# Performance work log

Measured on AMD Instinct MI355X. Metric: run time of the kernel, lower is better.

Reference implementation:

```python
import jax, jax.numpy as jnp
import numpy as np

N = 50000      # nodes
E = 800000     # edges
F = 128        # num_features
H = 128        # hidden_channels
L = 3          # num_layers
P = 32         # num_partitions
EPS = 1e-5     # BatchNorm1d eps


def _batchnorm(h):
    # BatchNorm1d(affine=False, track_running_stats=False): batch stats, biased var
    m = jnp.mean(h, axis=0)
    v = jnp.var(h, axis=0)
    return (h - m) * jax.lax.rsqrt(v + EPS)


def setup_inputs() -> dict:
    key = jax.random.key(0)
    ks = jax.random.split(key, 12)
    x = jax.random.normal(ks[0], (N, F), dtype=jnp.float32)
    edge_index = jax.random.randint(ks[1], (2, E), 0, N)
    edge_weights = jax.random.uniform(ks[2], (E,), dtype=jnp.float32)
    partitions = (jax.random.uniform(ks[3], (N, P)) < (1.0 / P)).astype(jnp.float32)
    node_weights = jax.random.uniform(ks[4], (N,), dtype=jnp.float32)
    edge_curr_node = jax.random.uniform(ks[5], (N,), dtype=jnp.float32)
    conv_w = 0.05 * jax.random.normal(ks[6], (L, F, H), dtype=jnp.float32)
    conv_b = jnp.zeros((L, H), dtype=jnp.float32)
    lin1_w = 0.05 * jax.random.normal(ks[7], (4 * H, H), dtype=jnp.float32)
    lin1_b = jnp.zeros((H,), dtype=jnp.float32)
    lin2_w = 0.05 * jax.random.normal(ks[8], (H, 1), dtype=jnp.float32)
    lin2_b = jnp.zeros((1,), dtype=jnp.float32)
    return {"x": x, "edge_index": edge_index, "edge_weights": edge_weights,
            "partitions": partitions, "node_weights": node_weights,
            "edge_curr_node": edge_curr_node, "conv_w": conv_w, "conv_b": conv_b,
            "lin1_w": lin1_w, "lin1_b": lin1_b, "lin2_w": lin2_w,
            "lin2_b": lin2_b, "curr_node_id": 123}


def reference(x, edge_index, edge_weights, partitions, node_weights,
              edge_curr_node, conv_w, conv_b, lin1_w, lin1_b, lin2_w, lin2_b,
              curr_node_id):
    src, dst = edge_index[0], edge_index[1]
    # GCN normalization with added self-loops (weight 1)
    deg = jax.ops.segment_sum(edge_weights, dst, num_segments=N) + 1.0
    dinv = jax.lax.rsqrt(deg)
    norm = dinv[src] * edge_weights * dinv[dst]          # [E]
    self_norm = (dinv * dinv)[:, None]                   # [N,1]

    h = x
    for l in range(L):
        hw = h @ conv_w[l] + conv_b[l]                   # [N,H]
        agg = jax.ops.segment_sum(hw[src] * norm[:, None], dst, num_segments=N)
        agg = agg + hw * self_norm                       # self-loop term
        h = jax.nn.relu(_batchnorm(agg))

    x_curr = h[curr_node_id]                             # [H]
    # mlp scoring: concat [h | x_curr | edge_col repeated to 2H] -> [N,4H]
    cat = jnp.concatenate([
        h,
        jnp.broadcast_to(x_curr[None, :], (N, H)),
        jnp.broadcast_to(edge_curr_node[:, None], (N, 2 * H)),
    ], axis=1)
    scores = jax.nn.relu(cat @ lin1_w + lin1_b) @ lin2_w + lin2_b  # [N,1]
    # pool == 'sum'
    partition_scores = scores.T @ partitions             # [1,P]
    return (partition_scores, h)
```

## Files before the change

kernel.cpp:

```cpp
#include <hip/hip_runtime.h>

#define N_NODES 50000
#define N_EDGES 800000
#define NP 50048
#define BKT 784
#define NBKT 64
#define BREG 16384
#define HB 782
#define PADK 136
#define NCOPY 64
#define WPB 512

typedef __bf16 bf16_8 __attribute__((ext_vector_type(8)));
typedef float  f32_4  __attribute__((ext_vector_type(4)));

__device__ inline float2 bf2f2(unsigned int u) {
    union { unsigned int i; float f; } a, b;
    a.i = u << 16;
    b.i = u & 0xffff0000u;
    return make_float2(a.f, b.f);
}

__global__ void k_init_wprep(float* __restrict__ colpart, float* __restrict__ out_head,
                             int* __restrict__ cursor,
                             const float* __restrict__ conv_w, const float* __restrict__ lin1_w,
                             __bf16* __restrict__ WT, float* __restrict__ svec) {
    int b = blockIdx.x;
    if (b < 64) {
        int i = b * 256 + threadIdx.x;
        colpart[i] = 0.f;
        if (i < 32) out_head[i] = 0.f;
        if (i < NBKT) cursor[i] = 0;
    } else if (b < 64 + WPB) {
        int b2 = b - 64;
        int mat = b2 >> 7, n = b2 & 127, k = threadIdx.x;
        if (k < 128) {
            const float* srcm = (mat < 3) ? (conv_w + (size_t)mat * 16384) : lin1_w;
            WT[((size_t)mat * 128 + n) * 128 + k] = (__bf16)srcm[(size_t)k * 128 + n];
        }
    } else {
        int j = threadIdx.x;
        if (j < 128) {
            float s = 0.f;
            for (int k = 256; k < 512; ++k) s += lin1_w[(size_t)k * 128 + j];
            svec[j] = s;
        }
    }
}

__global__ __launch_bounds__(256) void k_scatter(const int* __restrict__ src,
                                                 const int* __restrict__ dst,
                                                 const float* __restrict__ ew,
                                                 int* __restrict__ cursor,
                                                 uint2* __restrict__ ebuf) {
    __shared__ int c[NBKT], basee[NBKT];
    int t = threadIdx.x, b = blockIdx.x;
    if (t < NBKT) c[t] = 0;
    __syncthreads();
    int e0 = b * 1024;
    int myd[4], mybkt[4];
#pragma unroll
    for (int j = 0; j < 4; ++j) {
        int e = e0 + t + j * 256;
        mybkt[j] = -1;
        if (e < N_EDGES) {
            myd[j] = dst[e];
            mybkt[j] = myd[j] / BKT;
            atomicAdd(&c[mybkt[j]], 1);
        }
    }
    __syncthreads();
    if (t < NBKT && c[t] > 0) basee[t] = atomicAdd(&cursor[t], c[t]);
    __syncthreads();
    if (t < NBKT) c[t] = 0;
    __syncthreads();
#pragma unroll
    for (int j = 0; j < 4; ++j) {
        if (mybkt[j] >= 0) {
            int e = e0 + t + j * 256;
            int bkt = mybkt[j];
            int dl = myd[j] - bkt * BKT;
            int pos = basee[bkt] + atomicAdd(&c[bkt], 1);
            ebuf[(size_t)bkt * BREG + pos] =
                make_uint2(((unsigned)dl << 17) | (unsigned)src[e], __float_as_uint(ew[e]));
        }
    }
}

__global__ __launch_bounds__(256) void k_build(const uint2* __restrict__ ebuf,
                                               const int* __restrict__ cursor,
                                               uint2* __restrict__ esn2,
                                               int* __restrict__ offs, int* __restrict__ cnt,
                                               float* __restrict__ dinv) {
    __shared__ int   c784[1024];
    __shared__ float deg784[1024];
    __shared__ int   o784[1024];
    __shared__ int   fill784[1024];
    __shared__ int   p[256];
    int b = blockIdx.x, t = threadIdx.x;
    size_t base = (size_t)b * BREG;
    int num = cursor[b];
    for (int i = t; i < 1024; i += 256) { c784[i] = 0; deg784[i] = 1.0f; fill784[i] = 0; }
    __syncthreads();
    for (int i = t; i < num; i += 256) {
        uint2 eu = ebuf[base + i];
        int dl = eu.x >> 17;
        atomicAdd(&c784[dl], 1);
        atomicAdd(&deg784[dl], __uint_as_float(eu.y));
    }
    __syncthreads();
    for (int i = t; i < BKT; i += 256) deg784[i] = rsqrtf(deg784[i]);
    int s0 = c784[4 * t] + c784[4 * t + 1] + c784[4 * t + 2] + c784[4 * t + 3];
    p[t] = s0;
    __syncthreads();
    int own = s0;
    for (int d = 1; d < 256; d <<= 1) {
        int v = (t >= d) ? p[t - d] : 0;
        __syncthreads();
        p[t] += v;
        __syncthreads();
    }
    int e0 = p[t] - own;
    o784[4 * t] = e0;
    o784[4 * t + 1] = e0 + c784[4 * t];
    o784[4 * t + 2] = e0 + c784[4 * t] + c784[4 * t + 1];
    o784[4 * t + 3] = e0 + c784[4 * t] + c784[4 * t + 1] + c784[4 * t + 2];
    __syncthreads();
    int nb0 = b * BKT;
    for (int i = t; i < BKT; i += 256) {
        int n = nb0 + i;
        if (n < N_NODES) {
            offs[n] = (int)base + o784[i];
            cnt[n] = c784[i];
            dinv[n] = deg784[i];
        }
    }
    __syncthreads();
    for (int i = t; i < num; i += 256) {
        uint2 eu = ebuf[base + i];
        int dl = eu.x >> 17;
        int s  = (int)(eu.x & 131071u);
        int pos = (int)base + o784[dl] + atomicAdd(&fill784[dl], 1);
        esn2[pos] = make_uint2((unsigned)s,
                               __float_as_uint(__uint_as_float(eu.y) * deg784[dl]));
    }
}

template <int AMODE>
__global__ __launch_bounds__(256) void k_gemm_mfma(const float* __restrict__ A,
                                                   const float* __restrict__ mean,
                                                   const float* __restrict__ rstd,
                                                   const __bf16* __restrict__ WT,
                                                   const float* __restrict__ bias,
                                                   __bf16* __restrict__ C, int nrows) {
    __shared__ __bf16 As[64 * PADK];
    __shared__ __bf16 Ws[128 * PADK];
    int t = threadIdx.x;
    int rowBase = blockIdx.x * 64;
    const uint4* WTg = (const uint4*)WT;
    for (int i = t; i < 2048; i += 256) {
        int n = i >> 4, k8 = i & 15;
        *(uint4*)&Ws[n * PADK + k8 * 8] = WTg[i];
    }
    const float4* A4 = (const float4*)A;
    const float4* M4 = (const float4*)mean;
    const float4* R4 = (const float4*)rstd;
    for (int i = t; i < 1024; i += 256) {
        int r = i >> 4, k8 = i & 15;
        int gr = rowBase + r;
        float4 a0 = make_float4(0.f, 0.f, 0.f, 0.f), a1 = a0;
        if (gr < nrows) {
            a0 = A4[(size_t)gr * 32 + k8 * 2];
            a1 = A4[(size_t)gr * 32 + k8 * 2 + 1];
        }
        if (AMODE == 1) {
            float4 m0 = M4[k8 * 2], m1 = M4[k8 * 2 + 1];
            float4 r0 = R4[k8 * 2], r1 = R4[k8 * 2 + 1];
            a0.x = fmaxf((a0.x - m0.x) * r0.x, 0.f); a0.y = fmaxf((a0.y - m0.y) * r0.y, 0.f);
            a0.z = fmaxf((a0.z - m0.z) * r0.z, 0.f); a0.w = fmaxf((a0.w - m0.w) * r0.w, 0.f);
            a1.x = fmaxf((a1.x - m1.x) * r1.x, 0.f); a1.y = fmaxf((a1.y - m1.y) * r1.y, 0.f);
            a1.z = fmaxf((a1.z - m1.z) * r1.z, 0.f); a1.w = fmaxf((a1.w - m1.w) * r1.w, 0.f);
        }
        bf16_8 o = { (__bf16)a0.x, (__bf16)a0.y, (__bf16)a0.z, (__bf16)a0.w,
                     (__bf16)a1.x, (__bf16)a1.y, (__bf16)a1.z, (__bf16)a1.w };
        *(bf16_8*)&As[r * PADK + k8 * 8] = o;
    }
    __syncthreads();
    int wave = t >> 6, lane = t & 63, quad = lane >> 4, m = lane & 15;
    int ar = wave * 16 + m;
    f32_4 acc[8];
#pragma unroll
    for (int i = 0; i < 8; ++i) acc[i] = (f32_4){0.f, 0.f, 0.f, 0.f};
#pragma unroll
    for (int kk = 0; kk < 4; ++kk) {
        bf16_8 a = *(const bf16_8*)&As[ar * PADK + kk * 32 + quad * 8];
#pragma unroll
        for (int n0 = 0; n0 < 8; ++n0) {
            bf16_8 b = *(const bf16_8*)&Ws[(n0 * 16 + m) * PADK + kk * 32 + quad * 8];
            acc[n0] = __builtin_amdgcn_mfma_f32_16x16x32_bf16(a, b, acc[n0], 0, 0, 0);
        }
    }
    __syncthreads();
#pragma unroll
    for (int n0 = 0; n0 < 8; ++n0) {
        int col = n0 * 16 + m;
        float bi = bias[col];
#pragma unroll
        for (int r = 0; r < 4; ++r) {
            int rr = wave * 16 + quad * 4 + r;
            As[rr * PADK + col] = (__bf16)(acc[n0][r] + bi);
        }
    }
    __syncthreads();
    uint4* Cg = (uint4*)C;
    for (int i = t; i < 1024; i += 256) {
        int r = i >> 4, k8 = i & 15;
        int gr = rowBase + r;
        if (gr < nrows) Cg[(size_t)gr * 16 + k8] = *(const uint4*)&As[r * PADK + k8 * 8];
    }
}

__global__ __launch_bounds__(256) void k_agg(const __bf16* __restrict__ hwb,
                                             const uint2* __restrict__ esn2,
                                             const int* __restrict__ offs,
                                             const int* __restrict__ cnt,
                                             const float* __restrict__ dinv,
                                             float* __restrict__ agg,
                                             float* __restrict__ colpart) {
    __shared__ float red1[4 * 128], red2[4 * 128];
    int t = threadIdx.x;
    int n = (blockIdx.x * 256 + t) >> 6;
    int lane = t & 63, wave = t >> 6;
    float2 acc = make_float2(0.f, 0.f);
    const unsigned int* hw32 = (const unsigned int*)hwb;
    if (n < N_NODES) {
        float dvn = dinv[n];
        float2 sv = bf2f2(hw32[(size_t)n * 64 + lane]);
        acc.x = sv.x * dvn * dvn; acc.y = sv.y * dvn * dvn;
        int beg = offs[n], num = cnt[n];
        for (int ch = 0; ch < num; ch += 64) {
            int nn = min(64, num - ch);
            int s_l = 0; float w_l = 0.f;
            if (lane < nn) {
                uint2 e = esn2[beg + ch + lane];
                s_l = (int)e.x;
                w_l = dinv[s_l] * __uint_as_float(e.y);
            }
            int i = 0;
            for (; i + 8 <= nn; i += 8) {
                int ss[8]; float ww[8]; unsigned uu[8];
#pragma unroll
                for (int j = 0; j < 8; ++j) { ss[j] = __shfl(s_l, i + j); ww[j] = __shfl(w_l, i + j); }
#pragma unroll
                for (int j = 0; j < 8; ++j) uu[j] = hw32[(size_t)ss[j] * 64 + lane];
#pragma unroll
                for (int j = 0; j < 8; ++j) {
                    float2 f = bf2f2(uu[j]);
                    acc.x += f.x * ww[j]; acc.y += f.y * ww[j];
                }
            }
            for (; i < nn; ++i) {
                int s = __shfl(s_l, i);
                float w = __shfl(w_l, i);
                float2 f = bf2f2(hw32[(size_t)s * 64 + lane]);
                acc.x += f.x * w; acc.y += f.y * w;
            }
        }
        ((float2*)agg)[(size_t)n * 64 + lane] = acc;
    }
    *(float2*)&red1[wave * 128 + 2 * lane] = acc;
    *(float2*)&red2[wave * 128 + 2 * lane] = make_float2(acc.x * acc.x, acc.y * acc.y);
    __syncthreads();
    if (t < 128) {
        float s = red1[t] + red1[128 + t] + red1[256 + t] + red1[384 + t];
        float q = red2[t] + red2[128 + t] + red2[256 + t] + red2[384 + t];
        int c = blockIdx.x & (NCOPY - 1);
        unsafeAtomicAdd(&colpart[c * 128 + t], s);
        unsafeAtomicAdd(&colpart[NCOPY * 128 + c * 128 + t], q);
    }
}

template <int DO_PREP>
__global__ void k_bnfinal(float* __restrict__ colpart, float* __restrict__ mean,
                          float* __restrict__ rstd,
                          const float* __restrict__ agg, const int* __restrict__ cid,
                          const float* __restrict__ lin1w, const float* __restrict__ lin1b,
                          float* __restrict__ c0) {
    __shared__ float s1[256], s2[256], ms[128], rs[128], xc[128];
    int t = threadIdx.x;
    int j = t & 127, g = t >> 7;
    float s = 0.f, q = 0.f;
    for (int c = g * 32; c < g * 32 + 32; ++c) {
        s += colpart[c * 128 + j];
        q += colpart[NCOPY * 128 + c * 128 + j];
        colpart[c * 128 + j] = 0.f;
        colpart[NCOPY * 128 + c * 128 + j] = 0.f;
    }
    s1[t] = s; s2[t] = q;
    __syncthreads();
    if (t < 128) {
        float S = s1[t] + s1[t + 128];
        float Q = s2[t] + s2[t + 128];
        float m = S * (1.0f / N_NODES);
        float v = Q * (1.0f / N_NODES) - m * m;
        float r = rsqrtf(v + 1e-5f);
        mean[t] = m; rstd[t] = r;
        if (DO_PREP) { ms[t] = m; rs[t] = r; }
    }
    if (DO_PREP) {
        __syncthreads();
        int cn = cid[0];
        if (t < 128) xc[t] = fmaxf((agg[(size_t)cn * 128 + t] - ms[t]) * rs[t], 0.f);
        __syncthreads();
        float acc = g ? 0.f : lin1b[j];
        for (int k = g * 64; k < g * 64 + 64; ++k)
            acc += xc[k] * lin1w[(size_t)(128 + k) * 128 + j];
        s1[t] = acc;
        __syncthreads();
        if (t < 128) c0[t] = s1[t] + s1[t + 128];
    }
}

__global__ __launch_bounds__(256) void k_score_mfma(const float* __restrict__ agg,
                                                    const float* __restrict__ mean,
                                                    const float* __restrict__ rstd,
                                                    const __bf16* __restrict__ WT,
                                                    const float* __restrict__ c0,
                                                    const float* __restrict__ svec,
                                                    const float* __restrict__ ecn,
                                                    const float* __restrict__ lin2w,
                                                    const float* __restrict__ lin2b,
                                                    const float* __restrict__ part,
                                                    float* __restrict__ out,
                                                    float* __restrict__ hout,
                                                    int nrows) {
    __shared__ __bf16 As[64 * PADK];
    __shared__ __bf16 Ws[128 * PADK];
    __shared__ float c0s[128], svs[128], l2s[128];
    __shared__ float sc[64], red[256];
    int t = threadIdx.x;
    int rowBase = blockIdx.x * 64;
    const uint4* WTg = (const uint4*)WT;
    for (int i = t; i < 2048; i += 256) {
        int n = i >> 4, k8 = i & 15;
        *(uint4*)&Ws[n * PADK + k8 * 8] = WTg[i];
    }
    const float4* A4 = (const float4*)agg;
    const float4* M4 = (const float4*)mean;
    const float4* R4 = (const float4*)rstd;
    float4* H4 = (float4*)hout;
    for (int i = t; i < 1024; i += 256) {
        int r = i >> 4, k8 = i & 15;
        int gr = rowBase + r;
        float4 a0 = make_float4(0.f, 0.f, 0.f, 0.f), a1 = a0;
        if (gr < nrows) {
            a0 = A4[(size_t)gr * 32 + k8 * 2];
            a1 = A4[(size_t)gr * 32 + k8 * 2 + 1];
        }
        float4 m0 = M4[k8 * 2], m1 = M4[k8 * 2 + 1];
        float4 r0 = R4[k8 * 2], r1 = R4[k8 * 2 + 1];
        float4 f0, f1;
        f0.x = fmaxf((a0.x - m0.x) * r0.x, 0.f); f0.y = fmaxf((a0.y - m0.y) * r0.y, 0.f);
        f0.z = fmaxf((a0.z - m0.z) * r0.z, 0.f); f0.w = fmaxf((a0.w - m0.w) * r0.w, 0.f);
        f1.x = fmaxf((a1.x - m1.x) * r1.x, 0.f); f1.y = fmaxf((a1.y - m1.y) * r1.y, 0.f);
        f1.z = fmaxf((a1.z - m1.z) * r1.z, 0.f); f1.w = fmaxf((a1.w - m1.w) * r1.w, 0.f);
        if (gr < nrows) {
            H4[(size_t)gr * 32 + k8 * 2] = f0;
            H4[(size_t)gr * 32 + k8 * 2 + 1] = f1;
        }
        bf16_8 o = { (__bf16)f0.x, (__bf16)f0.y, (__bf16)f0.z, (__bf16)f0.w,
                     (__bf16)f1.x, (__bf16)f1.y, (__bf16)f1.z, (__bf16)f1.w };
        *(bf16_8*)&As[r * PADK + k8 * 8] = o;
    }
    if (t < 128) { c0s[t] = c0[t]; svs[t] = svec[t]; l2s[t] = lin2w[t]; }
    __syncthreads();
    int wave = t >> 6, lane = t & 63, quad = lane >> 4, m = lane & 15;
    int ar = wave * 16 + m;
    f32_4 acc[8];
#pragma unroll
    for (int i = 0; i < 8; ++i) acc[i] = (f32_4){0.f, 0.f, 0.f, 0.f};
#pragma unroll
    for (int kk = 0; kk < 4; ++kk) {
        bf16_8 a = *(const bf16_8*)&As[ar * PADK + kk * 32 + quad * 8];
#pragma unroll
        for (int n0 = 0; n0 < 8; ++n0) {
            bf16_8 b = *(const bf16_8*)&Ws[(n0 * 16 + m) * PADK + kk * 32 + quad * 8];
            acc[n0] = __builtin_amdgcn_mfma_f32_16x16x32_bf16(a, b, acc[n0], 0, 0, 0);
        }
    }
    float l2b = lin2b[0];
#pragma unroll
    for (int r = 0; r < 4; ++r) {
        int row = rowBase + wave * 16 + quad * 4 + r;
        float e = (row < nrows) ? ecn[row] : 0.f;
        float partial = 0.f;
#pragma unroll
        for (int n0 = 0; n0 < 8; ++n0) {
            int col = n0 * 16 + m;
            float v = acc[n0][r] + c0s[col] + e * svs[col];
            partial += fmaxf(v, 0.f) * l2s[col];
        }
        partial += __shfl_xor(partial, 8, 16);
        partial += __shfl_xor(partial, 4, 16);
        partial += __shfl_xor(partial, 2, 16);
        partial += __shfl_xor(partial, 1, 16);
        if (m == 0) sc[wave * 16 + quad * 4 + r] = partial + l2b;
    }
    __syncthreads();
    int rg = t >> 5, pp = t & 31;
    float a = 0.f;
    for (int j = 0; j < 8; ++j) {
        int r = rg * 8 + j;
        int row = rowBase + r;
        if (row < nrows) a += sc[r] * part[(size_t)row * 32 + pp];
    }
    red[t] = a;
    __syncthreads();
    if (t < 32) {
        float s = 0.f;
        for (int i = 0; i < 8; ++i) s += red[i * 32 + t];
        unsafeAtomicAdd(&out[t], s);
    }
}

extern "C" void kernel_launch(void* const* d_in, const int* in_sizes, int n_in,
                              void* d_out, int out_size, void* d_ws, size_t ws_size,
                              hipStream_t stream) {
    const float* x        = (const float*)d_in[0];
    const int*   eidx     = (const int*)d_in[1];
    const float* ew       = (const float*)d_in[2];
    const float* parts    = (const float*)d_in[3];
    const float* ecn      = (const float*)d_in[5];
    const float* conv_w   = (const float*)d_in[6];
    const float* conv_b   = (const float*)d_in[7];
    const float* lin1_w   = (const float*)d_in[8];
    const float* lin1_b   = (const float*)d_in[9];
    const float* lin2_w   = (const float*)d_in[10];
    const float* lin2_b   = (const float*)d_in[11];
    const int*   cid      = (const int*)d_in[12];

    const int* src = eidx;
    const int* dst = eidx + N_EDGES;

    char* p = (char*)d_ws;
    auto alloc = [&](size_t bytes) { char* r = p; p += (bytes + 255) & ~size_t(255); return r; };
    int*    cursor  = (int*)alloc(NBKT * 4);
    uint2*  ebuf    = (uint2*)alloc((size_t)NBKT * BREG * 8);
    uint2*  esn2    = (uint2*)alloc((size_t)NBKT * BREG * 8);
    int*    offs    = (int*)alloc(NP * 4);
    int*    cnt     = (int*)alloc(NP * 4);
    float*  dinv    = (float*)alloc(NP * 4);
    float*  colpart = (float*)alloc(2 * NCOPY * 128 * 4);
    float*  mean    = (float*)alloc(128 * 4);
    float*  rstd    = (float*)alloc(128 * 4);
    float*  c0      = (float*)alloc(128 * 4);
    float*  svec    = (float*)alloc(128 * 4);
    __bf16* WT      = (__bf16*)alloc(4 * 128 * 128 * 2);
    __bf16* hwb     = (__bf16*)alloc((size_t)N_NODES * 128 * 2);
    float*  agg     = (float*)alloc((size_t)N_NODES * 128 * 4);

    float* out_head = (float*)d_out;
    float* hbuf     = (float*)d_out + 32;

    const int GB = (N_NODES + 63) / 64;
    const int AB = (N_NODES * 64 + 255) / 256;

    k_init_wprep<<<64 + WPB + 1, 256, 0, stream>>>(colpart, out_head, cursor,
                                                   conv_w, lin1_w, WT, svec);
    k_scatter<<<HB, 256, 0, stream>>>(src, dst, ew, cursor, ebuf);
    k_build<<<NBKT, 256, 0, stream>>>(ebuf, cursor, esn2, offs, cnt, dinv);

    for (int l = 0; l < 3; ++l) {
        if (l == 0)
            k_gemm_mfma<0><<<GB, 256, 0, stream>>>(x, mean, rstd, WT, conv_b, hwb, N_NODES);
        else
            k_gemm_mfma<1><<<GB, 256, 0, stream>>>(agg, mean, rstd, WT + (size_t)l * 16384,
                                                   conv_b + (size_t)l * 128, hwb, N_NODES);
        k_agg<<<AB, 256, 0, stream>>>(hwb, esn2, offs, cnt, dinv, agg, colpart);
        if (l < 2)
            k_bnfinal<0><<<1, 256, 0, stream>>>(colpart, mean, rstd,
                                                agg, cid, lin1_w, lin1_b, c0);
        else
            k_bnfinal<1><<<1, 256, 0, stream>>>(colpart, mean, rstd,
                                                agg, cid, lin1_w, lin1_b, c0);
    }

    k_score_mfma<<<GB, 256, 0, stream>>>(agg, mean, rstd, WT + (size_t)3 * 16384, c0, svec,
                                         ecn, lin2_w, lin2_b, parts, out_head, hbuf, N_NODES);
}
```

Measured before the change: 373.5 us.

## Halve edge bucket size and stage sorted CSR edges in shared memory

Edges are now split into 128 destination buckets of 392 nodes instead of 64 of 784, which doubles the number of build blocks for more parallelism. The sorted edge records are staged in LDS and written to global memory in coalesced order instead of being scattered. The lin1 column-sum prep is split across two thread groups. Bucket overflow past BREG is now silently clamped, which drops edges if a bucket exceeds 8192 entries.

New measurement: 358.1 us. -4.1%, faster.

```diff
diff --git a/kernel.cpp b/kernel.cpp
--- a/kernel.cpp
+++ b/kernel.cpp
@@ -3,9 +3,10 @@
 #define N_NODES 50000
 #define N_EDGES 800000
 #define NP 50048
-#define BKT 784
-#define NBKT 64
-#define BREG 16384
+#define BKT 392
+#define NBKT 128
+#define BREG 8192
+#define SCAP 7168
 #define HB 782
 #define PADK 136
 #define NCOPY 64
@@ -39,12 +40,14 @@
             WT[((size_t)mat * 128 + n) * 128 + k] = (__bf16)srcm[(size_t)k * 128 + n];
         }
     } else {
-        int j = threadIdx.x;
-        if (j < 128) {
-            float s = 0.f;
-            for (int k = 256; k < 512; ++k) s += lin1_w[(size_t)k * 128 + j];
-            svec[j] = s;
-        }
+        __shared__ float sv[256];
+        int j = threadIdx.x & 127, g = threadIdx.x >> 7;
+        float s = 0.f;
+        for (int k = 256 + g * 128; k < 256 + g * 128 + 128; ++k)
+            s += lin1_w[(size_t)k * 128 + j];
+        sv[threadIdx.x] = s;
+        __syncthreads();
+        if (threadIdx.x < 128) svec[j] = sv[j] + sv[j + 128];
     }
 }
 
@@ -81,8 +84,9 @@
             int bkt = mybkt[j];
             int dl = myd[j] - bkt * BKT;
             int pos = basee[bkt] + atomicAdd(&c[bkt], 1);
-            ebuf[(size_t)bkt * BREG + pos] =
-                make_uint2(((unsigned)dl << 17) | (unsigned)src[e], __float_as_uint(ew[e]));
+            if (pos < BREG)
+                ebuf[(size_t)bkt * BREG + pos] =
+                    make_uint2(((unsigned)dl << 17) | (unsigned)src[e], __float_as_uint(ew[e]));
         }
     }
 }
@@ -92,25 +96,28 @@
                                                uint2* __restrict__ esn2,
                                                int* __restrict__ offs, int* __restrict__ cnt,
                                                float* __restrict__ dinv) {
-    __shared__ int   c784[1024];
-    __shared__ float deg784[1024];
-    __shared__ int   o784[1024];
-    __shared__ int   fill784[1024];
+    __shared__ uint2 stage[SCAP];
+    __shared__ int   cB[BKT];
+    __shared__ float degB[BKT];
+    __shared__ int   oB[BKT];
+    __shared__ int   fillB[BKT];
     __shared__ int   p[256];
     int b = blockIdx.x, t = threadIdx.x;
     size_t base = (size_t)b * BREG;
-    int num = cursor[b];
-    for (int i = t; i < 1024; i += 256) { c784[i] = 0; deg784[i] = 1.0f; fill784[i] = 0; }
+    int num = min(cursor[b], BREG);
+    for (int i = t; i < BKT; i += 256) { cB[i] = 0; degB[i] = 1.0f; fillB[i] = 0; }
     __syncthreads();
     for (int i = t; i < num; i += 256) {
         uint2 eu = ebuf[base + i];
         int dl = eu.x >> 17;
-        atomicAdd(&c784[dl], 1);
-        atomicAdd(&deg784[dl], __uint_as_float(eu.y));
-    }
-    __syncthreads();
-    for (int i = t; i < BKT; i += 256) deg784[i] = rsqrtf(deg784[i]);
-    int s0 = c784[4 * t] + c784[4 * t + 1] + c784[4 * t + 2] + c784[4 * t + 3];
+        atomicAdd(&cB[dl], 1);
+        atomicAdd(&degB[dl], __uint_as_float(eu.y));
+    }
+    __syncthreads();
+    for (int i = t; i < BKT; i += 256) degB[i] = rsqrtf(degB[i]);
+    int c0 = (2 * t     < BKT) ? cB[2 * t]     : 0;
+    int c1 = (2 * t + 1 < BKT) ? cB[2 * t + 1] : 0;
+    int s0 = c0 + c1;
     p[t] = s0;
     __syncthreads();
     int own = s0;
@@ -121,29 +128,32 @@
         __syncthreads();
     }
     int e0 = p[t] - own;
-    o784[4 * t] = e0;
-    o784[4 * t + 1] = e0 + c784[4 * t];
-    o784[4 * t + 2] = e0 + c784[4 * t] + c784[4 * t + 1];
-    o784[4 * t + 3] = e0 + c784[4 * t] + c784[4 * t + 1] + c784[4 * t + 2];
+    if (2 * t     < BKT) oB[2 * t]     = e0;
+    if (2 * t + 1 < BKT) oB[2 * t + 1] = e0 + c0;
     __syncthreads();
     int nb0 = b * BKT;
     for (int i = t; i < BKT; i += 256) {
         int n = nb0 + i;
         if (n < N_NODES) {
-            offs[n] = (int)base + o784[i];
-            cnt[n] = c784[i];
-            dinv[n] = deg784[i];
+            offs[n] = (int)base + oB[i];
+            cnt[n] = cB[i];
+            dinv[n] = degB[i];
         }
     }
     __syncthreads();
     for (int i = t; i < num; i += 256) {
         uint2 eu = ebuf[base + i];
         int dl = eu.x >> 17;
-        int s  = (int)(eu.x & 131071u);
-        int pos = (int)base + o784[dl] + atomicAdd(&fill784[dl], 1);
-        esn2[pos] = make_uint2((unsigned)s,
-                               __float_as_uint(__uint_as_float(eu.y) * deg784[dl]));
-    }
+        unsigned s = eu.x & 131071u;
+        int slot = oB[dl] + atomicAdd(&fillB[dl], 1);
+        uint2 val = make_uint2(s, __float_as_uint(__uint_as_float(eu.y) * degB[dl]));
+        if (slot < SCAP) stage[slot] = val;
+        else esn2[base + slot] = val;
+    }
+    __syncthreads();
+    int lim = min(num, SCAP);
+    for (int i = t; i < lim; i += 256)
+        esn2[base + i] = stage[i];
 }
 
 template <int AMODE>
```
